# Kernel optimization log

Measured on AMD Instinct MI355X. Metric: run time of the kernel, lower is better.

The kernel has to match this reference:

```python
import jax, jax.numpy as jnp
import numpy as np

N_NODES = 50000
N_EDGES = 600000
HID = 128
OUT = 14
LAYERS = 3
N_GRAPHS = 16
NODE_VOCAB = (120, 6)
EDGE_VOCAB = (6, 3)
GEN_EPS = 1e-7   # GENConv eps added after ReLU on messages
BN_EPS = 1e-5    # torch BatchNorm1d default eps


def setup_inputs() -> dict:
    key = jax.random.key(0)
    ks = jax.random.split(key, 14)
    inp = {}
    inp['node_feat0'] = jax.random.randint(ks[0], (N_NODES,), 0, NODE_VOCAB[0], dtype=jnp.int32)
    inp['node_feat1'] = jax.random.randint(ks[1], (N_NODES,), 0, NODE_VOCAB[1], dtype=jnp.int32)
    inp['edge_feat0'] = jax.random.randint(ks[2], (N_EDGES,), 0, EDGE_VOCAB[0], dtype=jnp.int32)
    inp['edge_feat1'] = jax.random.randint(ks[3], (N_EDGES,), 0, EDGE_VOCAB[1], dtype=jnp.int32)
    inp['edge_src'] = jax.random.randint(ks[4], (N_EDGES,), 0, N_NODES, dtype=jnp.int32)
    inp['edge_dst'] = jax.random.randint(ks[5], (N_EDGES,), 0, N_NODES, dtype=jnp.int32)
    inp['graph_ids'] = jnp.repeat(jnp.arange(N_GRAPHS, dtype=jnp.int32), N_NODES // N_GRAPHS)
    inp['num_graphs'] = N_GRAPHS
    s = 0.05
    inp['W_node0'] = jax.random.normal(ks[6], (NODE_VOCAB[0], HID), jnp.float32) * s
    inp['W_node1'] = jax.random.normal(ks[7], (NODE_VOCAB[1], HID), jnp.float32) * s
    # per-layer edge embedding tables (each GENConv layer has its own)
    inp['edge_emb0'] = jax.random.normal(ks[8], (LAYERS, EDGE_VOCAB[0], HID), jnp.float32) * s
    inp['edge_emb1'] = jax.random.normal(ks[9], (LAYERS, EDGE_VOCAB[1], HID), jnp.float32) * s
    inp['beta'] = jnp.ones((LAYERS,), jnp.float32)  # learnable softmax temperature, init 1.0
    inp['mlp_W'] = jax.random.normal(ks[10], (LAYERS, HID, HID), jnp.float32) * (1.0 / np.sqrt(HID))
    inp['mlp_b'] = jnp.zeros((LAYERS, HID), jnp.float32)
    inp['bn_gamma'] = jnp.ones((LAYERS, HID), jnp.float32)
    inp['bn_beta'] = jnp.zeros((LAYERS, HID), jnp.float32)
    inp['W_out'] = jax.random.normal(ks[11], (HID, OUT), jnp.float32) * (1.0 / np.sqrt(HID))
    inp['b_out'] = jnp.zeros((OUT,), jnp.float32)
    return inp


def _segment_softmax(z, seg, num_segments):
    # DGL edge_softmax: elementwise softmax over edges sharing a destination node.
    zmax = jax.ops.segment_max(z, seg, num_segments=num_segments)
    zmax = jnp.where(jnp.isfinite(zmax), zmax, 0.0)  # guard empty segments
    e = jnp.exp(z - zmax[seg])
    denom = jax.ops.segment_sum(e, seg, num_segments=num_segments)
    return e / denom[seg]


def reference(node_feat0, node_feat1, edge_feat0, edge_feat1, edge_src, edge_dst,
              graph_ids, num_graphs, W_node0, W_node1, edge_emb0, edge_emb1,
              beta, mlp_W, mlp_b, bn_gamma, bn_beta, W_out, b_out):
    # node embedding lookup + sum over tables
    hv = W_node0[node_feat0] + W_node1[node_feat1]          # [N, H]
    n = hv.shape[0]
    for l in range(mlp_W.shape[0]):
        # BatchNorm1d (training mode: batch stats, biased variance) + ReLU
        mu = jnp.mean(hv, axis=0)
        var = jnp.var(hv, axis=0)
        hv1 = (hv - mu) * jax.lax.rsqrt(var + BN_EPS) * bn_gamma[l] + bn_beta[l]
        hv1 = jax.nn.relu(hv1)
        # GENConv: edge embed sum, u_add_e, relu+eps, edge_softmax, scatter-sum
        ee = edge_emb0[l][edge_feat0] + edge_emb1[l][edge_feat1]   # [E, H]
        m = jax.nn.relu(hv1[edge_src] + ee) + GEN_EPS              # [E, H]
        a = _segment_softmax(m * beta[l], edge_dst, n)             # [E, H]
        agg = jax.ops.segment_sum(m * a, edge_dst, num_segments=n)  # [N, H]
        # feats = node_feats + msg, then 1-layer MLP, then outer skip connect
        hv = (hv1 + agg) @ mlp_W[l] + mlp_b[l] + hv
    # AvgPooling over each graph in the batch, then output Linear
    counts = jax.ops.segment_sum(jnp.ones((n,), hv.dtype), graph_ids, num_segments=num_graphs)
    hg = jax.ops.segment_sum(hv, graph_ids, num_segments=num_graphs) / counts[:, None]
    return hg @ W_out + b_out  # [num_graphs, OUT]
```

## Files before the change

### kernel.cpp

```cpp
#include <hip/hip_runtime.h>

#define N_NODESC 50000
#define N_EDGESC 600000
#define HID 128
#define LAYERS 3
#define N_GRAPHSC 16
#define OUT_DIM 14
#define GEN_EPS 1e-7f
#define BN_EPS 1e-5f
#define SCAN_BLK 196
#define EMB_BLK 6250
#define WF_BLK 192
#define CNT_BLK 2344
#define GEMM_BLK 782
#define BNR_BLK 64
#define LOG2E 1.44269504f

typedef short bf16x8 __attribute__((ext_vector_type(8)));
typedef float f32x4 __attribute__((ext_vector_type(4)));

__device__ __forceinline__ unsigned short f2bf(float f) {
    union { float f; unsigned u; } v; v.f = f;
    unsigned r = v.u + 0x7FFF + ((v.u >> 16) & 1);
    return (unsigned short)(r >> 16);
}
__device__ __forceinline__ float bf_lo(unsigned u) {
    return __uint_as_float(u << 16);
}
__device__ __forceinline__ float bf_hi(unsigned u) {
    return __uint_as_float(u & 0xFFFF0000u);
}
__device__ __forceinline__ float bfs(unsigned short u) {
    return __uint_as_float(((unsigned)u) << 16);
}

__global__ void k_blocksum(const int* __restrict__ deg, int* __restrict__ part) {
    __shared__ int sh[256];
    int t = threadIdx.x;
    int i = blockIdx.x * 256 + t;
    sh[t] = (i < N_NODESC) ? deg[i] : 0;
    __syncthreads();
    for (int off = 128; off > 0; off >>= 1) {
        if (t < off) sh[t] += sh[t + off];
        __syncthreads();
    }
    if (t == 0) part[blockIdx.x] = sh[0];
}

__global__ void k_scanpart(const int* __restrict__ part, int* __restrict__ bofs) {
    __shared__ int sh[256];
    int t = threadIdx.x;
    int v = (t < SCAN_BLK) ? part[t] : 0;
    sh[t] = v;
    __syncthreads();
    for (int off = 1; off < 256; off <<= 1) {
        int add = (t >= off) ? sh[t - off] : 0;
        __syncthreads();
        sh[t] += add;
        __syncthreads();
    }
    if (t < SCAN_BLK) bofs[t] = sh[t] - v;
}

__global__ void k_rowptr(const int* __restrict__ deg, const int* __restrict__ bofs,
                         int* __restrict__ row_ptr, int* __restrict__ cursor) {
    __shared__ int sh[256];
    int t = threadIdx.x;
    int i = blockIdx.x * 256 + t;
    int d = (i < N_NODESC) ? deg[i] : 0;
    sh[t] = d;
    __syncthreads();
    for (int off = 1; off < 256; off <<= 1) {
        int add = (t >= off) ? sh[t - off] : 0;
        __syncthreads();
        sh[t] += add;
        __syncthreads();
    }
    if (i < N_NODESC) {
        int rp = bofs[blockIdx.x] + sh[t] - d;
        row_ptr[i] = rp;
        cursor[i] = rp;
    }
    if (i == 0) row_ptr[N_NODESC] = N_EDGESC;
}

__global__ void k_scatter(const int* __restrict__ dst, const int* __restrict__ src,
                          const int* __restrict__ f0, const int* __restrict__ f1,
                          int* __restrict__ cursor, int* __restrict__ csr_pack) {
    int i = blockIdx.x * blockDim.x + threadIdx.x;
    if (i < N_EDGESC) {
        int pos = atomicAdd(&cursor[dst[i]], 1);
        csr_pack[pos] = (src[i] << 8) | ((f0[i] * 3 + f1[i]) * 8);
    }
}

__global__ void k_embed(const int* __restrict__ f0, const int* __restrict__ f1,
                        const float4* __restrict__ W0, const float4* __restrict__ W1,
                        uint2* __restrict__ hvb2, float* __restrict__ part,
                        const float* __restrict__ W, unsigned short* __restrict__ wf,
                        const int* __restrict__ edst, int* __restrict__ deg) {
    int tid = threadIdx.x;
    if (blockIdx.x >= EMB_BLK + WF_BLK) {
        int e = (blockIdx.x - EMB_BLK - WF_BLK) * 256 + tid;
        if (e < N_EDGESC) atomicAdd(&deg[edst[e]], 1);
        return;
    }
    if (blockIdx.x >= EMB_BLK) {
        int i = (blockIdx.x - EMB_BLK) * 256 + tid;
        if (i < LAYERS * 16384) {
            int j = i & 7;
            int lane = (i >> 3) & 63;
            int nt = (i >> 9) & 7;
            int ks = (i >> 12) & 3;
            int l = i >> 14;
            int k = ks * 32 + (lane >> 4) * 8 + j;
            int n = nt * 16 + (lane & 15);
            wf[i] = f2bf(W[(size_t)l * HID * HID + k * HID + n]);
        }
        return;
    }
    __shared__ float sh[1024], sh2[1024];
    int i = blockIdx.x * 256 + tid;
    int v = i >> 5, c4 = i & 31;
    float4 a = W0[f0[v] * 32 + c4];
    float4 b = W1[f1[v] * 32 + c4];
    float4 o = make_float4(a.x + b.x, a.y + b.y, a.z + b.z, a.w + b.w);
    uint2 ob;
    ob.x = (unsigned)f2bf(o.x) | ((unsigned)f2bf(o.y) << 16);
    ob.y = (unsigned)f2bf(o.z) | ((unsigned)f2bf(o.w) << 16);
    hvb2[i] = ob;
    sh[tid * 4 + 0] = o.x; sh2[tid * 4 + 0] = o.x * o.x;
    sh[tid * 4 + 1] = o.y; sh2[tid * 4 + 1] = o.y * o.y;
    sh[tid * 4 + 2] = o.z; sh2[tid * 4 + 2] = o.z * o.z;
    sh[tid * 4 + 3] = o.w; sh2[tid * 4 + 3] = o.w * o.w;
    __syncthreads();
    if (tid < 128) {
        int c4i = tid >> 2, j = tid & 3;
        float s = 0.f, s2 = 0.f;
#pragma unroll
        for (int r = 0; r < 8; r++) {
            s += sh[(r * 32 + c4i) * 4 + j];
            s2 += sh2[(r * 32 + c4i) * 4 + j];
        }
        part[(size_t)blockIdx.x * 256 + tid] = s;
        part[(size_t)blockIdx.x * 256 + 128 + tid] = s2;
    }
}

__global__ void k_bn_reduce2(const float* __restrict__ part, int nparts,
                             float* __restrict__ gsum) {
    int t = threadIdx.x;
    int rows = (nparts + BNR_BLK - 1) / BNR_BLK;
    int r0 = blockIdx.x * rows;
    int r1 = min(r0 + rows, nparts);
    float s = 0.f;
    for (int p = r0; p < r1; p++) s += part[(size_t)p * 256 + t];
    atomicAdd(&gsum[t], s);
}

__global__ __launch_bounds__(1024) void k_aggemm(
    const unsigned* __restrict__ hin, unsigned short* __restrict__ hout,
    const int* __restrict__ row_ptr, const int* __restrict__ csr_pack,
    const float* __restrict__ e0, const float* __restrict__ e1,
    const float* __restrict__ beta_p, const unsigned short* __restrict__ wf,
    const float* __restrict__ b, const float* __restrict__ gsum,
    const float* __restrict__ gamma, const float* __restrict__ betab,
    float* __restrict__ gsum_next, float* __restrict__ hg) {
    __shared__ float2 sh_et[18 * 64];
    __shared__ unsigned x_tile[64 * 64];
    __shared__ float shs[512], shs2[512];
    int tid = threadIdx.x;
    for (int i = tid; i < 18 * 64; i += 1024) {
        int f = i >> 6, ln = i & 63;
        int a = f / 3, bb = f - 3 * a;
        float2 ea = *(const float2*)(e0 + a * HID + 2 * ln);
        float2 eb = *(const float2*)(e1 + bb * HID + 2 * ln);
        sh_et[i] = make_float2(ea.x + eb.x, ea.y + eb.y);
    }
    int w = tid >> 6, lane = tid & 63;
    int m0 = blockIdx.x * 64;
    const float bl2 = (*beta_p) * LOG2E;
    const float invN = 1.f / (float)N_NODESC;
    int cch = lane * 2;
    float mu0 = gsum[cch] * invN, mu1 = gsum[cch + 1] * invN;
    float var0 = gsum[128 + cch] * invN - mu0 * mu0;
    float var1 = gsum[129 + cch] * invN - mu1 * mu1;
    float sc0 = gamma[cch] * rsqrtf(var0 + BN_EPS);
    float sc1 = gamma[cch + 1] * rsqrtf(var1 + BN_EPS);
    float sf0 = betab[cch] - mu0 * sc0;
    float sf1 = betab[cch + 1] - mu1 * sc1;
    __syncthreads();

    const char* hinc = (const char*)hin;
    const char* etc = (const char*)sh_et;
    unsigned lane4 = (unsigned)lane * 4;
    unsigned lane8 = (unsigned)lane * 8;

#define AGG_BODY(J)                                                         \
    {                                                                       \
        int pack = __shfl(pk, (J), 64);                                     \
        unsigned u = *(const unsigned*)(hinc +                              \
                        ((((unsigned)pack) & 0xFFFFFF00u) + lane4));        \
        float2 t = *(const float2*)(etc +                                   \
                        (((((unsigned)pack) & 0xFFu) << 6) + lane8));       \
        float a0 = fmaxf(fmaf(bf_lo(u), sc0, sf0), 0.f);                    \
        float a1 = fmaxf(fmaf(bf_hi(u), sc1, sf1), 0.f);                    \
        float r0 = fmaxf(a0 + t.x, 0.f);                                    \
        float r1 = fmaxf(a1 + t.y, 0.f);                                    \
        float w0 = exp2f(r0 * bl2);                                         \
        float w1 = exp2f(r1 * bl2);                                         \
        d0 += w0; d1 += w1;                                                 \
        n0 = fmaf(r0, w0, n0); n1 = fmaf(r1, w1, n1);                       \
    }

    for (int i = 0; i < 4; i++) {
        int row = w * 4 + i;
        int v = m0 + row;
        int vc = min(v, N_NODESC - 1);
        unsigned su = hin[(size_t)vc * 64 + lane];
        float h10 = fmaxf(fmaf(bf_lo(su), sc0, sf0), 0.f);
        float h11 = fmaxf(fmaf(bf_hi(su), sc1, sf1), 0.f);
        int p0 = row_ptr[vc];
        int deg = (v < N_NODESC) ? (row_ptr[vc + 1] - p0) : 0;
        float n0 = 0.f, n1 = 0.f, d0 = 0.f, d1 = 0.f;
        for (int base = 0; base < deg; base += 64) {
            int idx = base + lane;
            int pk = (idx < deg) ? csr_pack[p0 + idx] : 0;
            int jn = min(64, deg - base);
            int j = 0;
            for (; j + 2 <= jn; j += 2) {
                AGG_BODY(j)
                AGG_BODY(j + 1)
            }
            if (j < jn) AGG_BODY(j)
        }
        float ox = h10 + (deg ? __fdividef(n0, d0) + GEN_EPS : 0.f);
        float oy = h11 + (deg ? __fdividef(n1, d1) + GEN_EPS : 0.f);
        x_tile[row * 64 + ((lane + row * 4) & 63)] =
            (unsigned)f2bf(ox) | ((unsigned)f2bf(oy) << 16);
    }
#undef AGG_BODY
    __syncthreads();

    int rw = w & 3, chh = w >> 2;
    int mrow = lane & 15, grp = lane >> 4;
    int rbase = rw * 16 + mrow;
    bf16x8 af[4];
#pragma unroll
    for (int ks = 0; ks < 4; ks++) {
        int col = ks * 16 + grp * 4;
        int colr = (col + rbase * 4) & 63;
        af[ks] = *(const bf16x8*)&x_tile[rbase * 64 + colr];
    }
    f32x4 acc[2];
#pragma unroll
    for (int nt = 0; nt < 2; nt++) acc[nt] = (f32x4){0.f, 0.f, 0.f, 0.f};
#pragma unroll
    for (int nt = 0; nt < 2; nt++) {
        int ntg = chh * 2 + nt;
#pragma unroll
        for (int ks = 0; ks < 4; ks++) {
            bf16x8 bfr = *(const bf16x8*)(wf +
                (size_t)((ks * 8 + ntg) * 64 + lane) * 8);
            acc[nt] = __builtin_amdgcn_mfma_f32_16x16x32_bf16(
                af[ks], bfr, acc[nt], 0, 0, 0);
        }
    }
    const unsigned short* hin_s = (const unsigned short*)hin;
    int gA = m0 / 3125;
    int boundary = (gA + 1) * 3125;
#pragma unroll
    for (int nt = 0; nt < 2; nt++) {
        int col = chh * 32 + nt * 16 + mrow;
        float bias = b[col];
        float s = 0.f, s2 = 0.f;
#pragma unroll
        for (int r = 0; r < 4; r++) {
            int v = m0 + rw * 16 + grp * 4 + r;
            if (v < N_NODESC) {
                size_t idx = (size_t)v * HID + col;
                float o = acc[nt][r] + bias + bfs(hin_s[idx]);
                hout[idx] = f2bf(o);
                if (hg) {
                    if (v < boundary) s += o; else s2 += o;
                } else {
                    s += o; s2 += o * o;
                }
            }
        }
        s  += __shfl_xor(s, 16, 64);  s  += __shfl_xor(s, 32, 64);
        s2 += __shfl_xor(s2, 16, 64); s2 += __shfl_xor(s2, 32, 64);
        if (lane < 16) { shs[rw * 128 + col] = s; shs2[rw * 128 + col] = s2; }
    }
    __syncthreads();
    if (hg) {
        int gB = min(m0 + 63, N_NODESC - 1) / 3125;
        if (tid < 128) {
            atomicAdd(&hg[gA * 128 + tid],
                shs[tid] + shs[128 + tid] + shs[256 + tid] + shs[384 + tid]);
        } else if (tid < 256 && gB != gA) {
            int c = tid - 128;
            atomicAdd(&hg[gB * 128 + c],
                shs2[c] + shs2[128 + c] + shs2[256 + c] + shs2[384 + c]);
        }
    } else if (gsum_next) {
        if (tid < 128) {
            atomicAdd(&gsum_next[tid],
                shs[tid] + shs[128 + tid] + shs[256 + tid] + shs[384 + tid]);
        } else if (tid < 256) {
            int c = tid - 128;
            atomicAdd(&gsum_next[tid],
                shs2[c] + shs2[128 + c] + shs2[256 + c] + shs2[384 + c]);
        }
    }
}

__global__ void k_finish(const float* __restrict__ hg, const float* __restrict__ Wo,
                         const float* __restrict__ bo, float* __restrict__ out) {
    int t = threadIdx.x;
    if (t >= N_GRAPHSC * OUT_DIM) return;
    int g = t / OUT_DIM, o = t % OUT_DIM;
    const float inv = (float)N_GRAPHSC / (float)N_NODESC;
    float acc = bo[o];
    for (int k = 0; k < HID; k++)
        acc += hg[g * HID + k] * inv * Wo[k * OUT_DIM + o];
    out[t] = acc;
}

extern "C" void kernel_launch(void* const* d_in, const int* in_sizes, int n_in,
                              void* d_out, int out_size, void* d_ws, size_t ws_size,
                              hipStream_t stream) {
    const int* node_feat0 = (const int*)d_in[0];
    const int* node_feat1 = (const int*)d_in[1];
    const int* edge_feat0 = (const int*)d_in[2];
    const int* edge_feat1 = (const int*)d_in[3];
    const int* edge_src   = (const int*)d_in[4];
    const int* edge_dst   = (const int*)d_in[5];
    const float* W_node0   = (const float*)d_in[8];
    const float* W_node1   = (const float*)d_in[9];
    const float* edge_emb0 = (const float*)d_in[10];
    const float* edge_emb1 = (const float*)d_in[11];
    const float* beta      = (const float*)d_in[12];
    const float* mlp_W     = (const float*)d_in[13];
    const float* mlp_b     = (const float*)d_in[14];
    const float* bn_gamma  = (const float*)d_in[15];
    const float* bn_beta   = (const float*)d_in[16];
    const float* W_out     = (const float*)d_in[17];
    const float* b_out     = (const float*)d_in[18];
    float* out = (float*)d_out;

    char* ws = (char*)d_ws;
    size_t off = 0;
    auto alloc = [&](size_t bytes) -> void* {
        void* p = ws + off;
        off += (bytes + 255) & ~(size_t)255;
        return p;
    };
    unsigned short* hvA = (unsigned short*)alloc((size_t)N_NODESC * HID * 2);
    unsigned short* hvB = (unsigned short*)alloc((size_t)N_NODESC * HID * 2);
    float* gsums   = (float*)alloc(LAYERS * 256 * 4);
    float* hg      = (float*)alloc(N_GRAPHSC * HID * 4);
    float* bnpart  = (float*)alloc((size_t)EMB_BLK * 256 * 4);
    unsigned short* wfrag = (unsigned short*)alloc((size_t)LAYERS * 16384 * 2);
    int* row_ptr   = (int*)alloc((N_NODESC + 1) * 4);
    int* cursor    = (int*)alloc(N_NODESC * 4);
    int* deg       = (int*)alloc(N_NODESC * 4);
    int* part      = (int*)alloc(SCAN_BLK * 4);
    int* bofs      = (int*)alloc(SCAN_BLK * 4);
    int* csr_pack  = (int*)alloc((size_t)N_EDGESC * 4);

    hipMemsetAsync(deg, 0, N_NODESC * 4, stream);
    hipMemsetAsync(gsums, 0, LAYERS * 256 * 4 + N_GRAPHSC * HID * 4, stream);

    k_embed<<<EMB_BLK + WF_BLK + CNT_BLK, 256, 0, stream>>>(
        node_feat0, node_feat1, (const float4*)W_node0, (const float4*)W_node1,
        (uint2*)hvA, bnpart, mlp_W, wfrag, edge_dst, deg);

    k_blocksum<<<SCAN_BLK, 256, 0, stream>>>(deg, part);
    k_scanpart<<<1, 256, 0, stream>>>(part, bofs);
    k_rowptr<<<SCAN_BLK, 256, 0, stream>>>(deg, bofs, row_ptr, cursor);
    k_scatter<<<(N_EDGESC + 255) / 256, 256, 0, stream>>>(
        edge_dst, edge_src, edge_feat0, edge_feat1, cursor, csr_pack);

    k_bn_reduce2<<<BNR_BLK, 256, 0, stream>>>(bnpart, EMB_BLK, gsums);

    unsigned short* hin = hvA;
    unsigned short* hout = hvB;
    for (int l = 0; l < LAYERS; l++) {
        float* gsum = gsums + l * 256;
        float* gnext = (l + 1 < LAYERS) ? gsums + (l + 1) * 256 : nullptr;
        float* hgp = (l == LAYERS - 1) ? hg : nullptr;
        k_aggemm<<<GEMM_BLK, 1024, 0, stream>>>(
            (const unsigned*)hin, hout, row_ptr, csr_pack,
            edge_emb0 + (size_t)l * 6 * HID, edge_emb1 + (size_t)l * 3 * HID,
            beta + l, wfrag + (size_t)l * 16384, mlp_b + l * HID,
            gsum, bn_gamma + l * HID, bn_beta + l * HID, gnext, hgp);
        unsigned short* tmp = hin; hin = hout; hout = tmp;
    }

    k_finish<<<1, 256, 0, stream>>>(hg, W_out, b_out, out);
}
```

Before: 408.7 us.

## Stage block edge lists in LDS, batch gathers by four, dynamic row scheduling

```diff
diff --git a/kernel.cpp b/kernel.cpp
--- a/kernel.cpp
+++ b/kernel.cpp
@@ -14,6 +14,7 @@
 #define CNT_BLK 2344
 #define GEMM_BLK 782
 #define BNR_BLK 64
+#define EDGE_CAP 1792
 #define LOG2E 1.44269504f
 
 typedef short bf16x8 __attribute__((ext_vector_type(8)));
@@ -169,6 +170,9 @@
     __shared__ float2 sh_et[18 * 64];
     __shared__ unsigned x_tile[64 * 64];
     __shared__ float shs[512], shs2[512];
+    __shared__ int sh_pack[EDGE_CAP];
+    __shared__ int sh_rp[65];
+    __shared__ int row_ctr;
     int tid = threadIdx.x;
     for (int i = tid; i < 18 * 64; i += 1024) {
         int f = i >> 6, ln = i & 63;
@@ -179,6 +183,13 @@
     }
     int w = tid >> 6, lane = tid & 63;
     int m0 = blockIdx.x * 64;
+    if (tid < 65) sh_rp[tid] = row_ptr[min(m0 + tid, N_NODESC)];
+    if (tid == 0) row_ctr = 0;
+    int eb0 = row_ptr[m0];
+    int eb1 = row_ptr[min(m0 + 64, N_NODESC)];
+    int nE = min(eb1 - eb0, EDGE_CAP);
+    for (int i = tid; i < nE; i += 1024) sh_pack[i] = csr_pack[eb0 + i];
+
     const float bl2 = (*beta_p) * LOG2E;
     const float invN = 1.f / (float)N_NODESC;
     int cch = lane * 2;
@@ -196,50 +207,71 @@
     unsigned lane4 = (unsigned)lane * 4;
     unsigned lane8 = (unsigned)lane * 8;
 
-#define AGG_BODY(J)                                                         \
+#define GATH(S, PK)                                                         \
+    unsigned u##S = *(const unsigned*)(hinc +                               \
+                        ((((unsigned)(PK)) & 0xFFFFFF00u) + lane4));        \
+    float2 t##S = *(const float2*)(etc +                                    \
+                        (((((unsigned)(PK)) & 0xFFu) << 6) + lane8));
+#define CMP(S, VAL)                                                         \
     {                                                                       \
-        int pack = __shfl(pk, (J), 64);                                     \
-        unsigned u = *(const unsigned*)(hinc +                              \
-                        ((((unsigned)pack) & 0xFFFFFF00u) + lane4));        \
-        float2 t = *(const float2*)(etc +                                   \
-                        (((((unsigned)pack) & 0xFFu) << 6) + lane8));       \
-        float a0 = fmaxf(fmaf(bf_lo(u), sc0, sf0), 0.f);                    \
-        float a1 = fmaxf(fmaf(bf_hi(u), sc1, sf1), 0.f);                    \
-        float r0 = fmaxf(a0 + t.x, 0.f);                                    \
-        float r1 = fmaxf(a1 + t.y, 0.f);                                    \
-        float w0 = exp2f(r0 * bl2);                                         \
-        float w1 = exp2f(r1 * bl2);                                         \
+        float a0 = fmaxf(fmaf(bf_lo(u##S), sc0, sf0), 0.f);                 \
+        float a1 = fmaxf(fmaf(bf_hi(u##S), sc1, sf1), 0.f);                 \
+        float r0 = fmaxf(a0 + t##S.x, 0.f);                                 \
+        float r1 = fmaxf(a1 + t##S.y, 0.f);                                 \
+        float ei0 = (VAL) ? (r0 * bl2) : -1000.f;                           \
+        float ei1 = (VAL) ? (r1 * bl2) : -1000.f;                           \
+        float w0 = exp2f(ei0);                                              \
+        float w1 = exp2f(ei1);                                              \
         d0 += w0; d1 += w1;                                                 \
         n0 = fmaf(r0, w0, n0); n1 = fmaf(r1, w1, n1);                       \
     }
-
-    for (int i = 0; i < 4; i++) {
-        int row = w * 4 + i;
+#define EDGE_LOOP(SRC)                                                      \
+    for (int j0 = 0; j0 < deg; j0 += 4) {                                   \
+        int i0 = p0 + j0;                                                   \
+        int pkA = SRC(i0);                                                  \
+        int pkB = SRC(min(i0 + 1, last));                                   \
+        int pkC = SRC(min(i0 + 2, last));                                   \
+        int pkD = SRC(min(i0 + 3, last));                                   \
+        GATH(A, pkA) GATH(B, pkB) GATH(C, pkC) GATH(D, pkD)                 \
+        int rem = deg - j0;                                                 \
+        CMP(A, true)                                                        \
+        CMP(B, rem > 1)                                                     \
+        CMP(C, rem > 2)                                                     \
+        CMP(D, rem > 3)                                                     \
+    }
+#define SRC_LDS(I) sh_pack[(I)]
+#define SRC_GLB(I) csr_pack[eb0 + (I)]
+
+    for (;;) {
+        int rsel = 0;
+        if (lane == 0) rsel = atomicAdd(&row_ctr, 1);
+        rsel = __builtin_amdgcn_readfirstlane(rsel);
+        if (rsel >= 64) break;
+        int row = rsel;
         int v = m0 + row;
         int vc = min(v, N_NODESC - 1);
         unsigned su = hin[(size_t)vc * 64 + lane];
         float h10 = fmaxf(fmaf(bf_lo(su), sc0, sf0), 0.f);
         float h11 = fmaxf(fmaf(bf_hi(su), sc1, sf1), 0.f);
-        int p0 = row_ptr[vc];
-        int deg = (v < N_NODESC) ? (row_ptr[vc + 1] - p0) : 0;
+        int p0 = sh_rp[row] - eb0;
+        int deg = sh_rp[row + 1] - sh_rp[row];
+        int last = p0 + deg - 1;
         float n0 = 0.f, n1 = 0.f, d0 = 0.f, d1 = 0.f;
-        for (int base = 0; base < deg; base += 64) {
-            int idx = base + lane;
-            int pk = (idx < deg) ? csr_pack[p0 + idx] : 0;
-            int jn = min(64, deg - base);
-            int j = 0;
-            for (; j + 2 <= jn; j += 2) {
-                AGG_BODY(j)
-                AGG_BODY(j + 1)
-            }
-            if (j < jn) AGG_BODY(j)
+        if (p0 + deg <= nE) {
+            EDGE_LOOP(SRC_LDS)
+        } else {
+            EDGE_LOOP(SRC_GLB)
         }
         float ox = h10 + (deg ? __fdividef(n0, d0) + GEN_EPS : 0.f);
         float oy = h11 + (deg ? __fdividef(n1, d1) + GEN_EPS : 0.f);
         x_tile[row * 64 + ((lane + row * 4) & 63)] =
             (unsigned)f2bf(ox) | ((unsigned)f2bf(oy) << 16);
     }
-#undef AGG_BODY
+#undef EDGE_LOOP
+#undef GATH
+#undef CMP
+#undef SRC_LDS
+#undef SRC_GLB
     __syncthreads();
 
     int rw = w & 3, chh = w >> 2;
```

Measured after the change: 383.0 us. 1.07x faster.
